# Optimization experiments

Hardware: AMD Instinct MI355X
Metric: run time of the kernel (lower is better)

The kernel has to match this reference:

```python
import jax, jax.numpy as jnp
import numpy as np

B, C, W, H = 4, 256, 64, 64
DK = 32


def setup_inputs() -> dict:
    key = jax.random.key(0)
    ks = jax.random.split(key, 5)
    x = jax.random.normal(ks[0], (B, C, W, H), dtype=jnp.float32)
    # 1x1 conv weights ~ linear projections; scale like conv default init
    s = 1.0 / np.sqrt(C)
    Wq = jax.random.normal(ks[1], (DK, C), dtype=jnp.float32) * s
    Wk = jax.random.normal(ks[2], (DK, C), dtype=jnp.float32) * s
    Wv = jax.random.normal(ks[3], (C, C), dtype=jnp.float32) * s
    bq = jnp.zeros((DK,), jnp.float32)
    bk = jnp.zeros((DK,), jnp.float32)
    bv = jnp.zeros((C,), jnp.float32)
    # NOTE: module initializes gamma=0 (output == x, zero grads to Q/K/V);
    # use a nonzero value so the attention path is exercised.
    gamma = jax.random.uniform(ks[4], (1,), dtype=jnp.float32) + 0.5
    return {"x": x, "Wq": Wq, "bq": bq, "Wk": Wk, "bk": bk,
            "Wv": Wv, "bv": bv, "gamma": gamma}


def reference(x, Wq, bq, Wk, bk, Wv, bv, gamma):
    b, c, w, h = x.shape
    n = w * h
    xf = x.reshape(b, c, n)                      # [B, C, N]
    q = jnp.einsum('kc,bcn->bkn', Wq, xf) + bq[None, :, None]  # [B, dk, N]
    k = jnp.einsum('kc,bcn->bkn', Wk, xf) + bk[None, :, None]  # [B, dk, N]
    v = jnp.einsum('oc,bcn->bon', Wv, xf) + bv[None, :, None]  # [B, C, N]
    energy = jnp.einsum('bkn,bkm->bnm', q, k)    # [B, N, N] (no 1/sqrt(dk) scale)
    attn = jax.nn.softmax(energy, axis=-1)       # softmax over keys m
    # out[b,c,n] = sum_m v[b,c,m] * attn[b,n,m]  (bmm(V, A^T))
    out = jnp.einsum('bcm,bnm->bcn', v, attn)
    out = out.reshape(b, c, w, h)
    out = gamma[0] * out + x                      # channel_in == channel_out
    return out
```

## Files before the change

### kernel.cpp

```cpp
#include <hip/hip_runtime.h>
#include <hip/hip_bf16.h>
#include <stdint.h>

typedef float f32x16 __attribute__((ext_vector_type(16)));
typedef short bf16x8 __attribute__((ext_vector_type(8)));

#define L2E 1.4426950408889634f
#define ROWPAT(r, hi) (((r) & 3) + 8 * ((r) >> 2) + 4 * (hi))

#define WCATB_OFF 0u
#define QBUF_OFF  163840u
#define KBUF_OFF  1212416u
#define VBUF_OFF  2260992u

static __device__ __forceinline__ ushort f2bf(float f) {
    union { float f; uint32_t u; } v; v.f = f;
    uint32_t u = v.u;
    return (ushort)((u + 0x7fffu + ((u >> 16) & 1u)) >> 16);
}

static __device__ __forceinline__ uint32_t cvtpk(float lo, float hi) {
    uint32_t r;
    asm volatile("v_cvt_pk_bf16_f32 %0, %1, %2" : "=v"(r) : "v"(lo), "v"(hi));
    return r;
}
static __device__ __forceinline__ bf16x8 packP(float p0, float p1, float p2, float p3,
                                               float p4, float p5, float p6, float p7) {
    uint32_t a0 = cvtpk(p0, p1), a1 = cvtpk(p2, p3);
    uint32_t b0 = cvtpk(p4, p5), b1 = cvtpk(p6, p7);
    auto s0 = __builtin_amdgcn_permlane32_swap(a0, b0, false, false);
    auto s1 = __builtin_amdgcn_permlane32_swap(a1, b1, false, false);
    union { uint32_t u[4]; bf16x8 v; } pk;
    pk.u[0] = s0[0];
    pk.u[1] = s1[0];
    pk.u[2] = s0[1];
    pk.u[3] = s1[1];
    return pk.v;
}

__global__ void prep_kernel(const float* __restrict__ Wq, const float* __restrict__ Wk,
                            const float* __restrict__ Wv, ushort* __restrict__ Wcb) {
    int row = blockIdx.x, c = threadIdx.x;
    float v;
    if (row < 32)      v = Wq[row * 256 + c];
    else if (row < 64) v = Wk[(row - 32) * 256 + c];
    else               v = Wv[(row - 64) * 256 + c];
    Wcb[row * 256 + c] = f2bf(v);
}

__global__ __launch_bounds__(256)
void fproj_kernel(const float* __restrict__ x, const ushort* __restrict__ Wcb,
                  const float* __restrict__ bq, const float* __restrict__ bk,
                  const float* __restrict__ bv,
                  ushort* __restrict__ qbuf, ushort* __restrict__ kbuf,
                  ushort* __restrict__ vbuf) {
    __shared__ ushort xt[32 * 264];
    const int tid = threadIdx.x;
    const int b = blockIdx.x >> 7;
    const int n0 = (blockIdx.x & 127) << 5;

    const float* xb = x + (((size_t)b) << 20) + n0;
    #pragma unroll
    for (int i = 0; i < 8; ++i) {
        int task = tid + (i << 8);
        int c = task >> 3, seg = task & 7;
        float4 v = *(const float4*)(xb + (size_t)c * 4096 + seg * 4);
        xt[(seg * 4 + 0) * 264 + c] = f2bf(v.x);
        xt[(seg * 4 + 1) * 264 + c] = f2bf(v.y);
        xt[(seg * 4 + 2) * 264 + c] = f2bf(v.z);
        xt[(seg * 4 + 3) * 264 + c] = f2bf(v.w);
    }
    __syncthreads();

    const int w = tid >> 6, l = tid & 63;
    const int l31 = l & 31, hi = l >> 5;

    for (int cc = w; cc < 10; cc += 4) {
        const int wbase = (cc < 2) ? cc * 32 : (cc - 2) * 32 + 64;
        const ushort* wrow = Wcb + (size_t)(wbase + l31) * 256;
        f32x16 acc = (f32x16)0.0f;
        if (cc < 2) {
            #pragma unroll
            for (int kk = 0; kk < 16; ++kk) {
                bf16x8 xf = *(const bf16x8*)&xt[l31 * 264 + kk * 16 + hi * 8];
                bf16x8 wf = *(const bf16x8*)&wrow[kk * 16 + hi * 8];
                acc = __builtin_amdgcn_mfma_f32_32x32x16_bf16(xf, wf, acc, 0, 0, 0);
            }
            const float bias = (cc == 0) ? bq[l31] : bk[l31];
            const float scale = (cc == 0) ? L2E : 1.0f;
            ushort* dst = (cc == 0) ? qbuf : kbuf;
            #pragma unroll
            for (int r = 0; r < 16; ++r) {
                int n = n0 + ROWPAT(r, hi);
                dst[((size_t)((b << 12) + n)) * 32 + l31] = f2bf((acc[r] + bias) * scale);
            }
        } else {
            #pragma unroll
            for (int kk = 0; kk < 16; ++kk) {
                bf16x8 wf = *(const bf16x8*)&wrow[kk * 16 + hi * 8];
                bf16x8 xf = *(const bf16x8*)&xt[l31 * 264 + kk * 16 + hi * 8];
                acc = __builtin_amdgcn_mfma_f32_32x32x16_bf16(wf, xf, acc, 0, 0, 0);
            }
            #pragma unroll
            for (int r = 0; r < 16; ++r) {
                int c = (wbase - 64) + ROWPAT(r, hi);
                vbuf[((size_t)(b * 256 + c)) * 4096 + n0 + l31] = f2bf(acc[r] + bv[c]);
            }
        }
    }
}

#define KSTR 36
#define VSTR 66
__global__ __launch_bounds__(256, 2)
void attn_kernel(const ushort* __restrict__ qbuf, const ushort* __restrict__ kbuf,
                 const ushort* __restrict__ vbuf, const float* __restrict__ x,
                 const float* __restrict__ gammap, float* __restrict__ out) {
    __shared__ ushort klds[2][64 * KSTR];
    __shared__ ushort vlds[2][256 * VSTR];
    __shared__ float  dlds[2][2][32];

    const int tid = threadIdx.x;
    const int bid = blockIdx.x;
    const int work = (bid & 7) * 64 + (bid >> 3);
    const int b = work >> 7;
    const int qbase = (work & 127) << 5;
    const int w = tid >> 6, l = tid & 63;
    const int l31 = l & 31, hi = l >> 5;
    const int kh = w >> 1, cp = w & 1;
    const int cps = __builtin_amdgcn_readfirstlane(cp);

    const ushort* kb = kbuf + ((size_t)b << 12) * 32;
    const ushort* vb = vbuf + ((size_t)b << 8) * 4096;

    const ushort* qrow = qbuf + ((size_t)((b << 12) + qbase + l31)) * 32;
    const bf16x8 qf0 = *(const bf16x8*)&qrow[hi * 8];
    const bf16x8 qf1 = *(const bf16x8*)&qrow[16 + hi * 8];

    f32x16 acc[8];
    #pragma unroll
    for (int ch = 0; ch < 8; ++ch) acc[ch] = (f32x16)0.0f;
    float dsum = 0.f;

    const int vc = tid >> 3, vs = tid & 7;
    const int krow = tid >> 2, kseg = tid & 3;
    const ushort* vsrc = vb + (size_t)vc * 4096 + vs * 8;
    const ushort* ksrc = kb + (size_t)krow * 32 + kseg * 8;
    uint4 vreg[8], kreg;

    #pragma unroll
    for (int i = 0; i < 8; ++i)
        vreg[i] = *(const uint4*)(vsrc + (size_t)i * 32 * 4096);
    kreg = *(const uint4*)ksrc;
    #pragma unroll
    for (int i = 0; i < 8; ++i)
        *(uint4*)&vlds[0][(vc + 32 * i) * VSTR + vs * 8] = vreg[i];
    *(uint4*)&klds[0][krow * KSTR + kseg * 8] = kreg;
    __syncthreads();

    const int vcol = kh * 32 + cp * 16 + hi * 8;
    const int krow_a = (kh * 32 + l31) * KSTR;

    for (int it = 0; it < 64; ++it) {
        const int cur = it & 1;
        if (it < 63) {
            const size_t m0 = (size_t)(it + 1) << 6;
            #pragma unroll
            for (int i = 0; i < 8; ++i)
                vreg[i] = *(const uint4*)(vsrc + (size_t)i * 32 * 4096 + m0);
            kreg = *(const uint4*)(ksrc + (m0 << 5));
        }

        bf16x8 kf0 = *(const bf16x8*)&klds[cur][krow_a + hi * 8];
        bf16x8 kf1 = *(const bf16x8*)&klds[cur][krow_a + 16 + hi * 8];
        f32x16 sT = __builtin_amdgcn_mfma_f32_32x32x16_bf16(kf0, qf0, (f32x16)0.0f, 0, 0, 0);
        sT = __builtin_amdgcn_mfma_f32_32x32x16_bf16(kf1, qf1, sT, 0, 0, 0);

        float p[8];
        if (cps) {
            p[0] = exp2f(sT[8]);  p[1] = exp2f(sT[9]);  p[2] = exp2f(sT[10]); p[3] = exp2f(sT[11]);
            p[4] = exp2f(sT[12]); p[5] = exp2f(sT[13]); p[6] = exp2f(sT[14]); p[7] = exp2f(sT[15]);
        } else {
            p[0] = exp2f(sT[0]);  p[1] = exp2f(sT[1]);  p[2] = exp2f(sT[2]);  p[3] = exp2f(sT[3]);
            p[4] = exp2f(sT[4]);  p[5] = exp2f(sT[5]);  p[6] = exp2f(sT[6]);  p[7] = exp2f(sT[7]);
        }
        dsum += ((p[0] + p[1]) + (p[2] + p[3])) + ((p[4] + p[5]) + (p[6] + p[7]));
        bf16x8 pf = packP(p[0], p[1], p[2], p[3], p[4], p[5], p[6], p[7]);

        __builtin_amdgcn_s_setprio(1);
        #pragma unroll
        for (int ch = 0; ch < 8; ++ch) {
            bf16x8 vfa = *(const bf16x8*)&vlds[cur][(ch * 32 + l31) * VSTR + vcol];
            acc[ch] = __builtin_amdgcn_mfma_f32_32x32x16_bf16(vfa, pf, acc[ch], 0, 0, 0);
        }
        __builtin_amdgcn_s_setprio(0);

        if (it < 63) {
            const int nb = cur ^ 1;
            #pragma unroll
            for (int i = 0; i < 8; ++i)
                *(uint4*)&vlds[nb][(vc + 32 * i) * VSTR + vs * 8] = vreg[i];
            *(uint4*)&klds[nb][krow * KSTR + kseg * 8] = kreg;
        }
        __syncthreads();
    }

    const float gam = gammap[0];
    float dall = dsum + __shfl_xor(dsum, 32);
    if (l < 32) dlds[kh][cp][l31] = dall;
    float* scr = (float*)&vlds[0][0];
    __syncthreads();
    if (kh == 1) {
        #pragma unroll
        for (int ch = 0; ch < 8; ++ch)
            #pragma unroll
            for (int r = 0; r < 16; ++r)
                scr[(((cp * 8 + ch) * 16 + r) << 6) + l] = acc[ch][r];
    }
    __syncthreads();
    if (kh == 0) {
        #pragma unroll
        for (int ch = 0; ch < 8; ++ch)
            #pragma unroll
            for (int r = 0; r < 16; ++r)
                acc[ch][r] += scr[(((cp * 8 + ch) * 16 + r) << 6) + l];
    }
    __syncthreads();
    if (kh == 0 && cp == 1) {
        #pragma unroll
        for (int ch = 0; ch < 8; ++ch)
            #pragma unroll
            for (int r = 0; r < 16; ++r)
                scr[((ch * 16 + r) << 6) + l] = acc[ch][r];
    }
    __syncthreads();
    if (kh == 0 && cp == 0) {
        #pragma unroll
        for (int ch = 0; ch < 8; ++ch)
            #pragma unroll
            for (int r = 0; r < 16; ++r) {
                float o = acc[ch][r] + scr[((ch * 16 + r) << 6) + l];
                scr[((ch * 16 + r) << 6) + l] = o;
            }
    }
    __syncthreads();
    const float denom = dlds[0][0][l31] + dlds[0][1][l31] + dlds[1][0][l31] + dlds[1][1][l31];
    const float ginv = gam / denom;
    const float* xb2 = x + (((size_t)b) << 8) * 4096;
    float* ob = out + (((size_t)b) << 8) * 4096;
    const int q = qbase + l31;
    #pragma unroll
    for (int j = 0; j < 2; ++j) {
        const int ch = w * 2 + j;
        #pragma unroll
        for (int r = 0; r < 16; ++r) {
            int c = ch * 32 + ROWPAT(r, hi);
            float o = scr[((ch * 16 + r) << 6) + l];
            size_t idx = (size_t)c * 4096 + q;
            ob[idx] = o * ginv + xb2[idx];
        }
    }
}

extern "C" void kernel_launch(void* const* d_in, const int* in_sizes, int n_in,
                              void* d_out, int out_size, void* d_ws, size_t ws_size,
                              hipStream_t stream) {
    (void)in_sizes; (void)n_in; (void)out_size; (void)ws_size;
    const float* x     = (const float*)d_in[0];
    const float* Wq    = (const float*)d_in[1];
    const float* bq    = (const float*)d_in[2];
    const float* Wk    = (const float*)d_in[3];
    const float* bk    = (const float*)d_in[4];
    const float* Wv    = (const float*)d_in[5];
    const float* bv    = (const float*)d_in[6];
    const float* gamma = (const float*)d_in[7];
    float* out = (float*)d_out;

    char* ws = (char*)d_ws;
    ushort* Wcb  = (ushort*)(ws + WCATB_OFF);
    ushort* qbuf = (ushort*)(ws + QBUF_OFF);
    ushort* kbuf = (ushort*)(ws + KBUF_OFF);
    ushort* vbuf = (ushort*)(ws + VBUF_OFF);

    prep_kernel<<<320, 256, 0, stream>>>(Wq, Wk, Wv, Wcb);
    fproj_kernel<<<512, 256, 0, stream>>>(x, Wcb, bq, bk, bv, qbuf, kbuf, vbuf);
    attn_kernel<<<512, 256, 0, stream>>>(qbuf, kbuf, vbuf, x, gamma, out);
}
```

Measured before the change: 112.0 us.

## Load K/V MFMA fragments directly from global into registers, dropping LDS staging

The attention loop no longer stages K and V tiles through double-buffered shared memory with a block-wide barrier each iteration. Each wave now loads its own MFMA operand fragments straight from global memory into two register sets and alternates between them. This removes the LDS writes and reads and the per-iteration __syncthreads. In exchange, global loads become less coalesced (16-byte pieces strided across rows), data shared between waves is fetched redundantly, and register pressure rises, which may hurt the two-blocks-per-CU occupancy.

```diff
diff --git a/kernel.cpp b/kernel.cpp
--- a/kernel.cpp
+++ b/kernel.cpp
@@ -110,15 +110,12 @@
     }
 }
 
-#define KSTR 36
-#define VSTR 66
 __global__ __launch_bounds__(256, 2)
 void attn_kernel(const ushort* __restrict__ qbuf, const ushort* __restrict__ kbuf,
                  const ushort* __restrict__ vbuf, const float* __restrict__ x,
                  const float* __restrict__ gammap, float* __restrict__ out) {
-    __shared__ ushort klds[2][64 * KSTR];
-    __shared__ ushort vlds[2][256 * VSTR];
-    __shared__ float  dlds[2][2][32];
+    __shared__ float scr[16384];
+    __shared__ float dlds[2][2][32];
 
     const int tid = threadIdx.x;
     const int bid = blockIdx.x;
@@ -130,85 +127,86 @@
     const int kh = w >> 1, cp = w & 1;
     const int cps = __builtin_amdgcn_readfirstlane(cp);
 
-    const ushort* kb = kbuf + ((size_t)b << 12) * 32;
-    const ushort* vb = vbuf + ((size_t)b << 8) * 4096;
-
     const ushort* qrow = qbuf + ((size_t)((b << 12) + qbase + l31)) * 32;
     const bf16x8 qf0 = *(const bf16x8*)&qrow[hi * 8];
     const bf16x8 qf1 = *(const bf16x8*)&qrow[16 + hi * 8];
 
+    const ushort* kptr = kbuf + ((size_t)b << 12) * 32
+                       + (size_t)(kh * 32 + l31) * 32 + hi * 8;
+    const int vcol = kh * 32 + cp * 16 + hi * 8;
+    const ushort* vptr = vbuf + ((size_t)b << 8) * 4096
+                       + (size_t)l31 * 4096 + vcol;
+
     f32x16 acc[8];
     #pragma unroll
     for (int ch = 0; ch < 8; ++ch) acc[ch] = (f32x16)0.0f;
     float dsum = 0.f;
 
-    const int vc = tid >> 3, vs = tid & 7;
-    const int krow = tid >> 2, kseg = tid & 3;
-    const ushort* vsrc = vb + (size_t)vc * 4096 + vs * 8;
-    const ushort* ksrc = kb + (size_t)krow * 32 + kseg * 8;
-    uint4 vreg[8], kreg;
-
-    #pragma unroll
-    for (int i = 0; i < 8; ++i)
-        vreg[i] = *(const uint4*)(vsrc + (size_t)i * 32 * 4096);
-    kreg = *(const uint4*)ksrc;
-    #pragma unroll
-    for (int i = 0; i < 8; ++i)
-        *(uint4*)&vlds[0][(vc + 32 * i) * VSTR + vs * 8] = vreg[i];
-    *(uint4*)&klds[0][krow * KSTR + kseg * 8] = kreg;
-    __syncthreads();
-
-    const int vcol = kh * 32 + cp * 16 + hi * 8;
-    const int krow_a = (kh * 32 + l31) * KSTR;
-
-    for (int it = 0; it < 64; ++it) {
-        const int cur = it & 1;
-        if (it < 63) {
+    union u4bf { uint4 u; bf16x8 v; };
+    uint4 kA[2], kB[2], vA[8], vB[8];
+
+    kA[0] = *(const uint4*)(kptr);
+    kA[1] = *(const uint4*)(kptr + 16);
+    #pragma unroll
+    for (int ch = 0; ch < 8; ++ch)
+        vA[ch] = *(const uint4*)(vptr + (size_t)ch * 131072);
+
+#define ATTN_STEP(KR, VR)                                                          \
+    {                                                                              \
+        u4bf kf0, kf1;                                                             \
+        kf0.u = KR[0]; kf1.u = KR[1];                                              \
+        f32x16 sT = __builtin_amdgcn_mfma_f32_32x32x16_bf16(kf0.v, qf0,            \
+                                                            (f32x16)0.0f, 0, 0, 0);\
+        sT = __builtin_amdgcn_mfma_f32_32x32x16_bf16(kf1.v, qf1, sT, 0, 0, 0);     \
+        float p[8];                                                                \
+        if (cps) {                                                                 \
+            p[0] = exp2f(sT[8]);  p[1] = exp2f(sT[9]);                             \
+            p[2] = exp2f(sT[10]); p[3] = exp2f(sT[11]);                            \
+            p[4] = exp2f(sT[12]); p[5] = exp2f(sT[13]);                            \
+            p[6] = exp2f(sT[14]); p[7] = exp2f(sT[15]);                            \
+        } else {                                                                   \
+            p[0] = exp2f(sT[0]);  p[1] = exp2f(sT[1]);                             \
+            p[2] = exp2f(sT[2]);  p[3] = exp2f(sT[3]);                             \
+            p[4] = exp2f(sT[4]);  p[5] = exp2f(sT[5]);                             \
+            p[6] = exp2f(sT[6]);  p[7] = exp2f(sT[7]);                             \
+        }                                                                          \
+        dsum += ((p[0] + p[1]) + (p[2] + p[3])) + ((p[4] + p[5]) + (p[6] + p[7])); \
+        bf16x8 pf = packP(p[0], p[1], p[2], p[3], p[4], p[5], p[6], p[7]);         \
+        __builtin_amdgcn_s_setprio(1);                                             \
+        _Pragma("unroll")                                                          \
+        for (int ch = 0; ch < 8; ++ch) {                                           \
+            u4bf vf; vf.u = VR[ch];                                                \
+            acc[ch] = __builtin_amdgcn_mfma_f32_32x32x16_bf16(vf.v, pf,            \
+                                                              acc[ch], 0, 0, 0);   \
+        }                                                                          \
+        __builtin_amdgcn_s_setprio(0);                                             \
+    }
+
+    for (int it = 0; it < 64; it += 2) {
+        {
             const size_t m0 = (size_t)(it + 1) << 6;
-            #pragma unroll
-            for (int i = 0; i < 8; ++i)
-                vreg[i] = *(const uint4*)(vsrc + (size_t)i * 32 * 4096 + m0);
-            kreg = *(const uint4*)(ksrc + (m0 << 5));
-        }
-
-        bf16x8 kf0 = *(const bf16x8*)&klds[cur][krow_a + hi * 8];
-        bf16x8 kf1 = *(const bf16x8*)&klds[cur][krow_a + 16 + hi * 8];
-        f32x16 sT = __builtin_amdgcn_mfma_f32_32x32x16_bf16(kf0, qf0, (f32x16)0.0f, 0, 0, 0);
-        sT = __builtin_amdgcn_mfma_f32_32x32x16_bf16(kf1, qf1, sT, 0, 0, 0);
-
-        float p[8];
-        if (cps) {
-            p[0] = exp2f(sT[8]);  p[1] = exp2f(sT[9]);  p[2] = exp2f(sT[10]); p[3] = exp2f(sT[11]);
-            p[4] = exp2f(sT[12]); p[5] = exp2f(sT[13]); p[6] = exp2f(sT[14]); p[7] = exp2f(sT[15]);
-        } else {
-            p[0] = exp2f(sT[0]);  p[1] = exp2f(sT[1]);  p[2] = exp2f(sT[2]);  p[3] = exp2f(sT[3]);
-            p[4] = exp2f(sT[4]);  p[5] = exp2f(sT[5]);  p[6] = exp2f(sT[6]);  p[7] = exp2f(sT[7]);
-        }
-        dsum += ((p[0] + p[1]) + (p[2] + p[3])) + ((p[4] + p[5]) + (p[6] + p[7]));
-        bf16x8 pf = packP(p[0], p[1], p[2], p[3], p[4], p[5], p[6], p[7]);
-
-        __builtin_amdgcn_s_setprio(1);
-        #pragma unroll
-        for (int ch = 0; ch < 8; ++ch) {
-            bf16x8 vfa = *(const bf16x8*)&vlds[cur][(ch * 32 + l31) * VSTR + vcol];
-            acc[ch] = __builtin_amdgcn_mfma_f32_32x32x16_bf16(vfa, pf, acc[ch], 0, 0, 0);
-        }
-        __builtin_amdgcn_s_setprio(0);
-
-        if (it < 63) {
-            const int nb = cur ^ 1;
-            #pragma unroll
-            for (int i = 0; i < 8; ++i)
-                *(uint4*)&vlds[nb][(vc + 32 * i) * VSTR + vs * 8] = vreg[i];
-            *(uint4*)&klds[nb][krow * KSTR + kseg * 8] = kreg;
-        }
-        __syncthreads();
-    }
+            kB[0] = *(const uint4*)(kptr + m0 * 32);
+            kB[1] = *(const uint4*)(kptr + m0 * 32 + 16);
+            #pragma unroll
+            for (int ch = 0; ch < 8; ++ch)
+                vB[ch] = *(const uint4*)(vptr + (size_t)ch * 131072 + m0);
+        }
+        ATTN_STEP(kA, vA);
+        if (it < 62) {
+            const size_t m0 = (size_t)(it + 2) << 6;
+            kA[0] = *(const uint4*)(kptr + m0 * 32);
+            kA[1] = *(const uint4*)(kptr + m0 * 32 + 16);
+            #pragma unroll
+            for (int ch = 0; ch < 8; ++ch)
+                vA[ch] = *(const uint4*)(vptr + (size_t)ch * 131072 + m0);
+        }
+        ATTN_STEP(kB, vB);
+    }
+#undef ATTN_STEP
 
     const float gam = gammap[0];
     float dall = dsum + __shfl_xor(dsum, 32);
     if (l < 32) dlds[kh][cp][l31] = dall;
-    float* scr = (float*)&vlds[0][0];
     __syncthreads();
     if (kh == 1) {
         #pragma unroll
```

Result: slower. 163.9 us (+46.4%).

## Split attention channels across 8 waves per block to halve accumulators

Applied to the files above, without the earlier changes.

Moves the attention kernel from 4 to 8 waves per block. Each wave pair now covers half of the 256 output channels for a 16-key slice, so each wave holds 4 accumulator tiles instead of 8. V loads and the cross-wave reduction are reworked to match, and the final store is done straight from registers. Fewer registers per wave should raise occupancy and help hide latency. The cost is that the QK MFMA and exp work are repeated by more waves, and each iteration's block barrier now spans more waves.

```diff
diff --git a/kernel.cpp b/kernel.cpp
--- a/kernel.cpp
+++ b/kernel.cpp
@@ -112,13 +112,13 @@
 
 #define KSTR 36
 #define VSTR 66
-__global__ __launch_bounds__(256, 2)
+__global__ __launch_bounds__(512, 4)
 void attn_kernel(const ushort* __restrict__ qbuf, const ushort* __restrict__ kbuf,
                  const ushort* __restrict__ vbuf, const float* __restrict__ x,
                  const float* __restrict__ gammap, float* __restrict__ out) {
     __shared__ ushort klds[2][64 * KSTR];
     __shared__ ushort vlds[2][256 * VSTR];
-    __shared__ float  dlds[2][2][32];
+    __shared__ float  dlds[4][32];
 
     const int tid = threadIdx.x;
     const int bid = blockIdx.x;
@@ -127,38 +127,39 @@
     const int qbase = (work & 127) << 5;
     const int w = tid >> 6, l = tid & 63;
     const int l31 = l & 31, hi = l >> 5;
-    const int kh = w >> 1, cp = w & 1;
-    const int cps = __builtin_amdgcn_readfirstlane(cp);
-
-    const ushort* kb = kbuf + ((size_t)b << 12) * 32;
-    const ushort* vb = vbuf + ((size_t)b << 8) * 4096;
+    const int kq = w >> 1, chh = w & 1;
+    const int kh = kq >> 1;
+    const int kqo = kq & 1;
 
     const ushort* qrow = qbuf + ((size_t)((b << 12) + qbase + l31)) * 32;
     const bf16x8 qf0 = *(const bf16x8*)&qrow[hi * 8];
     const bf16x8 qf1 = *(const bf16x8*)&qrow[16 + hi * 8];
 
-    f32x16 acc[8];
-    #pragma unroll
-    for (int ch = 0; ch < 8; ++ch) acc[ch] = (f32x16)0.0f;
+    const ushort* kb = kbuf + ((size_t)b << 12) * 32;
+    const ushort* vb = vbuf + ((size_t)b << 8) * 4096;
+
+    f32x16 acc[4];
+    #pragma unroll
+    for (int ch = 0; ch < 4; ++ch) acc[ch] = (f32x16)0.0f;
     float dsum = 0.f;
 
     const int vc = tid >> 3, vs = tid & 7;
     const int krow = tid >> 2, kseg = tid & 3;
     const ushort* vsrc = vb + (size_t)vc * 4096 + vs * 8;
     const ushort* ksrc = kb + (size_t)krow * 32 + kseg * 8;
-    uint4 vreg[8], kreg;
-
-    #pragma unroll
-    for (int i = 0; i < 8; ++i)
-        vreg[i] = *(const uint4*)(vsrc + (size_t)i * 32 * 4096);
-    kreg = *(const uint4*)ksrc;
-    #pragma unroll
-    for (int i = 0; i < 8; ++i)
-        *(uint4*)&vlds[0][(vc + 32 * i) * VSTR + vs * 8] = vreg[i];
-    *(uint4*)&klds[0][krow * KSTR + kseg * 8] = kreg;
-    __syncthreads();
-
-    const int vcol = kh * 32 + cp * 16 + hi * 8;
+    uint4 vreg[4], kreg;
+
+    #pragma unroll
+    for (int i = 0; i < 4; ++i)
+        vreg[i] = *(const uint4*)(vsrc + (size_t)i * 64 * 4096);
+    if (tid < 256) kreg = *(const uint4*)ksrc;
+    #pragma unroll
+    for (int i = 0; i < 4; ++i)
+        *(uint4*)&vlds[0][(vc + 64 * i) * VSTR + vs * 8] = vreg[i];
+    if (tid < 256) *(uint4*)&klds[0][krow * KSTR + kseg * 8] = kreg;
+    __syncthreads();
+
+    const int vcol = kq * 16 + hi * 8;
     const int krow_a = (kh * 32 + l31) * KSTR;
 
     for (int it = 0; it < 64; ++it) {
@@ -166,9 +167,9 @@
         if (it < 63) {
             const size_t m0 = (size_t)(it + 1) << 6;
             #pragma unroll
-            for (int i = 0; i < 8; ++i)
-                vreg[i] = *(const uint4*)(vsrc + (size_t)i * 32 * 4096 + m0);
-            kreg = *(const uint4*)(ksrc + (m0 << 5));
+            for (int i = 0; i < 4; ++i)
+                vreg[i] = *(const uint4*)(vsrc + (size_t)i * 64 * 4096 + m0);
+            if (tid < 256) kreg = *(const uint4*)(ksrc + (m0 << 5));
         }
 
         bf16x8 kf0 = *(const bf16x8*)&klds[cur][krow_a + hi * 8];
@@ -177,7 +178,7 @@
         sT = __builtin_amdgcn_mfma_f32_32x32x16_bf16(kf1, qf1, sT, 0, 0, 0);
 
         float p[8];
-        if (cps) {
+        if (kqo) {
             p[0] = exp2f(sT[8]);  p[1] = exp2f(sT[9]);  p[2] = exp2f(sT[10]); p[3] = exp2f(sT[11]);
             p[4] = exp2f(sT[12]); p[5] = exp2f(sT[13]); p[6] = exp2f(sT[14]); p[7] = exp2f(sT[15]);
         } else {
@@ -189,75 +190,74 @@
 
         __builtin_amdgcn_s_setprio(1);
         #pragma unroll
-        for (int ch = 0; ch < 8; ++ch) {
-            bf16x8 vfa = *(const bf16x8*)&vlds[cur][(ch * 32 + l31) * VSTR + vcol];
-            acc[ch] = __builtin_amdgcn_mfma_f32_32x32x16_bf16(vfa, pf, acc[ch], 0, 0, 0);
+        for (int ch = 0; ch < 4; ++ch) {
+            bf16x8 vf = *(const bf16x8*)&vlds[cur][(chh * 128 + ch * 32 + l31) * VSTR + vcol];
+            acc[ch] = __builtin_amdgcn_mfma_f32_32x32x16_bf16(vf, pf, acc[ch], 0, 0, 0);
         }
         __builtin_amdgcn_s_setprio(0);
 
         if (it < 63) {
             const int nb = cur ^ 1;
             #pragma unroll
-            for (int i = 0; i < 8; ++i)
-                *(uint4*)&vlds[nb][(vc + 32 * i) * VSTR + vs * 8] = vreg[i];
-            *(uint4*)&klds[nb][krow * KSTR + kseg * 8] = kreg;
+            for (int i = 0; i < 4; ++i)
+                *(uint4*)&vlds[nb][(vc + 64 * i) * VSTR + vs * 8] = vreg[i];
+            if (tid < 256) *(uint4*)&klds[nb][krow * KSTR + kseg * 8] = kreg;
         }
         __syncthreads();
     }
 
     const float gam = gammap[0];
     float dall = dsum + __shfl_xor(dsum, 32);
-    if (l < 32) dlds[kh][cp][l31] = dall;
+    if (chh == 0 && l < 32) dlds[kq][l31] = dall;
     float* scr = (float*)&vlds[0][0];
     __syncthreads();
-    if (kh == 1) {
-        #pragma unroll
-        for (int ch = 0; ch < 8; ++ch)
-            #pragma unroll
-            for (int r = 0; r < 16; ++r)
-                scr[(((cp * 8 + ch) * 16 + r) << 6) + l] = acc[ch][r];
-    }
-    __syncthreads();
-    if (kh == 0) {
-        #pragma unroll
-        for (int ch = 0; ch < 8; ++ch)
-            #pragma unroll
-            for (int r = 0; r < 16; ++r)
-                acc[ch][r] += scr[(((cp * 8 + ch) * 16 + r) << 6) + l];
-    }
-    __syncthreads();
-    if (kh == 0 && cp == 1) {
-        #pragma unroll
-        for (int ch = 0; ch < 8; ++ch)
-            #pragma unroll
-            for (int r = 0; r < 16; ++r)
-                scr[((ch * 16 + r) << 6) + l] = acc[ch][r];
-    }
-    __syncthreads();
-    if (kh == 0 && cp == 0) {
-        #pragma unroll
-        for (int ch = 0; ch < 8; ++ch)
+    if (kqo) {
+        const int sb = (kh * 2 + chh) * 4;
+        #pragma unroll
+        for (int ch = 0; ch < 4; ++ch)
+            #pragma unroll
+            for (int r = 0; r < 16; ++r)
+                scr[(((sb + ch) * 16 + r) << 6) + l] = acc[ch][r];
+    }
+    __syncthreads();
+    if (!kqo) {
+        const int sb = (kh * 2 + chh) * 4;
+        #pragma unroll
+        for (int ch = 0; ch < 4; ++ch)
+            #pragma unroll
+            for (int r = 0; r < 16; ++r)
+                acc[ch][r] += scr[(((sb + ch) * 16 + r) << 6) + l];
+    }
+    __syncthreads();
+    if (kq == 2) {
+        const int sb = chh * 4;
+        #pragma unroll
+        for (int ch = 0; ch < 4; ++ch)
+            #pragma unroll
+            for (int r = 0; r < 16; ++r)
+                scr[(((sb + ch) * 16 + r) << 6) + l] = acc[ch][r];
+    }
+    __syncthreads();
+    if (kq == 0) {
+        const int sb = chh * 4;
+        #pragma unroll
+        for (int ch = 0; ch < 4; ++ch)
+            #pragma unroll
+            for (int r = 0; r < 16; ++r)
+                acc[ch][r] += scr[(((sb + ch) * 16 + r) << 6) + l];
+        const float denom = dlds[0][l31] + dlds[1][l31] + dlds[2][l31] + dlds[3][l31];
+        const float ginv = gam / denom;
+        const float* xb2 = x + (((size_t)b) << 8) * 4096;
+        float* ob = out + (((size_t)b) << 8) * 4096;
+        const int q = qbase + l31;
+        #pragma unroll
+        for (int ch = 0; ch < 4; ++ch) {
             #pragma unroll
             for (int r = 0; r < 16; ++r) {
-                float o = acc[ch][r] + scr[((ch * 16 + r) << 6) + l];
-                scr[((ch * 16 + r) << 6) + l] = o;
-            }
-    }
-    __syncthreads();
-    const float denom = dlds[0][0][l31] + dlds[0][1][l31] + dlds[1][0][l31] + dlds[1][1][l31];
-    const float ginv = gam / denom;
-    const float* xb2 = x + (((size_t)b) << 8) * 4096;
-    float* ob = out + (((size_t)b) << 8) * 4096;
-    const int q = qbase + l31;
-    #pragma unroll
-    for (int j = 0; j < 2; ++j) {
-        const int ch = w * 2 + j;
-        #pragma unroll
-        for (int r = 0; r < 16; ++r) {
-            int c = ch * 32 + ROWPAT(r, hi);
-            float o = scr[((ch * 16 + r) << 6) + l];
-            size_t idx = (size_t)c * 4096 + q;
-            ob[idx] = o * ginv + xb2[idx];
+                int c = chh * 128 + ch * 32 + ROWPAT(r, hi);
+                size_t idx = (size_t)c * 4096 + q;
+                ob[idx] = acc[ch][r] * ginv + xb2[idx];
+            }
         }
     }
 }
@@ -284,5 +284,5 @@
 
     prep_kernel<<<320, 256, 0, stream>>>(Wq, Wk, Wv, Wcb);
     fproj_kernel<<<512, 256, 0, stream>>>(x, Wcb, bq, bk, bv, qbuf, kbuf, vbuf);
-    attn_kernel<<<512, 256, 0, stream>>>(qbuf, kbuf, vbuf, x, gamma, out);
-}
+    attn_kernel<<<512, 512, 0, stream>>>(qbuf, kbuf, vbuf, x, gamma, out);
+}
```

Result: slower. 204.4 us (+82.5%).

## Split attention PV work by channel halves instead of key sub-slices per wave

Applied to the files above, without the earlier changes.

Each wave now computes all 16 score rows of its key half and exponentiates them, then accumulates a 128-channel half of the output using two MFMAs per channel tile, instead of every wave covering all 256 channels with 8 keys each. Accumulator registers drop from 8 to 4 tiles, and the cross-wave reduction shrinks from a four-way, multi-barrier LDS merge to a single two-way merge followed by the direct epilogue. The price is twice the exp2 work per wave, since waves with the same kh recompute the same probabilities, and a different LDS access pattern for V.

```diff
diff --git a/kernel.cpp b/kernel.cpp
--- a/kernel.cpp
+++ b/kernel.cpp
@@ -118,7 +118,7 @@
                  const float* __restrict__ gammap, float* __restrict__ out) {
     __shared__ ushort klds[2][64 * KSTR];
     __shared__ ushort vlds[2][256 * VSTR];
-    __shared__ float  dlds[2][2][32];
+    __shared__ float  dlds[2][32];
 
     const int tid = threadIdx.x;
     const int bid = blockIdx.x;
@@ -128,7 +128,6 @@
     const int w = tid >> 6, l = tid & 63;
     const int l31 = l & 31, hi = l >> 5;
     const int kh = w >> 1, cp = w & 1;
-    const int cps = __builtin_amdgcn_readfirstlane(cp);
 
     const ushort* kb = kbuf + ((size_t)b << 12) * 32;
     const ushort* vb = vbuf + ((size_t)b << 8) * 4096;
@@ -137,9 +136,9 @@
     const bf16x8 qf0 = *(const bf16x8*)&qrow[hi * 8];
     const bf16x8 qf1 = *(const bf16x8*)&qrow[16 + hi * 8];
 
-    f32x16 acc[8];
-    #pragma unroll
-    for (int ch = 0; ch < 8; ++ch) acc[ch] = (f32x16)0.0f;
+    f32x16 acc[4];
+    #pragma unroll
+    for (int ch = 0; ch < 4; ++ch) acc[ch] = (f32x16)0.0f;
     float dsum = 0.f;
 
     const int vc = tid >> 3, vs = tid & 7;
@@ -158,9 +157,6 @@
     *(uint4*)&klds[0][krow * KSTR + kseg * 8] = kreg;
     __syncthreads();
 
-    const int vcol = kh * 32 + cp * 16 + hi * 8;
-    const int krow_a = (kh * 32 + l31) * KSTR;
-
     for (int it = 0; it < 64; ++it) {
         const int cur = it & 1;
         if (it < 63) {
@@ -171,27 +167,29 @@
             kreg = *(const uint4*)(ksrc + (m0 << 5));
         }
 
+        const int krow_a = (kh * 32 + l31) * KSTR;
         bf16x8 kf0 = *(const bf16x8*)&klds[cur][krow_a + hi * 8];
         bf16x8 kf1 = *(const bf16x8*)&klds[cur][krow_a + 16 + hi * 8];
         f32x16 sT = __builtin_amdgcn_mfma_f32_32x32x16_bf16(kf0, qf0, (f32x16)0.0f, 0, 0, 0);
         sT = __builtin_amdgcn_mfma_f32_32x32x16_bf16(kf1, qf1, sT, 0, 0, 0);
 
-        float p[8];
-        if (cps) {
-            p[0] = exp2f(sT[8]);  p[1] = exp2f(sT[9]);  p[2] = exp2f(sT[10]); p[3] = exp2f(sT[11]);
-            p[4] = exp2f(sT[12]); p[5] = exp2f(sT[13]); p[6] = exp2f(sT[14]); p[7] = exp2f(sT[15]);
-        } else {
-            p[0] = exp2f(sT[0]);  p[1] = exp2f(sT[1]);  p[2] = exp2f(sT[2]);  p[3] = exp2f(sT[3]);
-            p[4] = exp2f(sT[4]);  p[5] = exp2f(sT[5]);  p[6] = exp2f(sT[6]);  p[7] = exp2f(sT[7]);
-        }
-        dsum += ((p[0] + p[1]) + (p[2] + p[3])) + ((p[4] + p[5]) + (p[6] + p[7]));
-        bf16x8 pf = packP(p[0], p[1], p[2], p[3], p[4], p[5], p[6], p[7]);
+        float p[16];
+        #pragma unroll
+        for (int r = 0; r < 16; ++r) {
+            p[r] = exp2f(sT[r]);
+            dsum += p[r];
+        }
+        bf16x8 pf0 = packP(p[0], p[1], p[2], p[3], p[4], p[5], p[6], p[7]);
+        bf16x8 pf1 = packP(p[8], p[9], p[10], p[11], p[12], p[13], p[14], p[15]);
 
         __builtin_amdgcn_s_setprio(1);
         #pragma unroll
-        for (int ch = 0; ch < 8; ++ch) {
-            bf16x8 vfa = *(const bf16x8*)&vlds[cur][(ch * 32 + l31) * VSTR + vcol];
-            acc[ch] = __builtin_amdgcn_mfma_f32_32x32x16_bf16(vfa, pf, acc[ch], 0, 0, 0);
+        for (int ch = 0; ch < 4; ++ch) {
+            const int crow = (cp * 128 + ch * 32 + l31) * VSTR + kh * 32;
+            bf16x8 vfa = *(const bf16x8*)&vlds[cur][crow + hi * 8];
+            bf16x8 vfb = *(const bf16x8*)&vlds[cur][crow + 16 + hi * 8];
+            acc[ch] = __builtin_amdgcn_mfma_f32_32x32x16_bf16(vfa, pf0, acc[ch], 0, 0, 0);
+            acc[ch] = __builtin_amdgcn_mfma_f32_32x32x16_bf16(vfb, pf1, acc[ch], 0, 0, 0);
         }
         __builtin_amdgcn_s_setprio(0);
 
@@ -207,57 +205,31 @@
 
     const float gam = gammap[0];
     float dall = dsum + __shfl_xor(dsum, 32);
-    if (l < 32) dlds[kh][cp][l31] = dall;
     float* scr = (float*)&vlds[0][0];
-    __syncthreads();
     if (kh == 1) {
         #pragma unroll
-        for (int ch = 0; ch < 8; ++ch)
+        for (int ch = 0; ch < 4; ++ch)
             #pragma unroll
             for (int r = 0; r < 16; ++r)
-                scr[(((cp * 8 + ch) * 16 + r) << 6) + l] = acc[ch][r];
-    }
+                scr[(((cp * 4 + ch) * 16 + r) << 6) + l] = acc[ch][r];
+    }
+    if (cp == 0 && l < 32) dlds[kh][l31] = dall;
     __syncthreads();
     if (kh == 0) {
-        #pragma unroll
-        for (int ch = 0; ch < 8; ++ch)
-            #pragma unroll
-            for (int r = 0; r < 16; ++r)
-                acc[ch][r] += scr[(((cp * 8 + ch) * 16 + r) << 6) + l];
-    }
-    __syncthreads();
-    if (kh == 0 && cp == 1) {
-        #pragma unroll
-        for (int ch = 0; ch < 8; ++ch)
-            #pragma unroll
-            for (int r = 0; r < 16; ++r)
-                scr[((ch * 16 + r) << 6) + l] = acc[ch][r];
-    }
-    __syncthreads();
-    if (kh == 0 && cp == 0) {
-        #pragma unroll
-        for (int ch = 0; ch < 8; ++ch)
+        const float denom = dlds[0][l31] + dlds[1][l31];
+        const float ginv = gam / denom;
+        const float* xb2 = x + (((size_t)b) << 8) * 4096;
+        float* ob = out + (((size_t)b) << 8) * 4096;
+        const int q = qbase + l31;
+        #pragma unroll
+        for (int ch = 0; ch < 4; ++ch) {
             #pragma unroll
             for (int r = 0; r < 16; ++r) {
-                float o = acc[ch][r] + scr[((ch * 16 + r) << 6) + l];
-                scr[((ch * 16 + r) << 6) + l] = o;
-            }
-    }
-    __syncthreads();
-    const float denom = dlds[0][0][l31] + dlds[0][1][l31] + dlds[1][0][l31] + dlds[1][1][l31];
-    const float ginv = gam / denom;
-    const float* xb2 = x + (((size_t)b) << 8) * 4096;
-    float* ob = out + (((size_t)b) << 8) * 4096;
-    const int q = qbase + l31;
-    #pragma unroll
-    for (int j = 0; j < 2; ++j) {
-        const int ch = w * 2 + j;
-        #pragma unroll
-        for (int r = 0; r < 16; ++r) {
-            int c = ch * 32 + ROWPAT(r, hi);
-            float o = scr[((ch * 16 + r) << 6) + l];
-            size_t idx = (size_t)c * 4096 + q;
-            ob[idx] = o * ginv + xb2[idx];
+                int c = cp * 128 + ch * 32 + ROWPAT(r, hi);
+                float o = acc[ch][r] + scr[(((cp * 4 + ch) * 16 + r) << 6) + l];
+                size_t idx = (size_t)c * 4096 + q;
+                ob[idx] = o * ginv + xb2[idx];
+            }
         }
     }
 }
```

After: 107.4 us. 4.1% less time.
